# Performance work log

Measured on AMD Instinct MI355X. Metric: run time of the kernel, lower is better.

## Reference

```python
import jax, jax.numpy as jnp
import numpy as np

NUM_BINS = 8
TAIL = 3.0
MBW = 0.001  # min_bin_width
MBH = 0.001  # min_bin_height
MD = 0.001   # min_derivative


def _conv(x, w, b):
    y = jax.lax.conv_general_dilated(x, w, (1, 1), 'SAME',
                                     dimension_numbers=('NCHW', 'OIHW', 'NCHW'))
    return y + b[None, :, None, None]


def _convnet(x, w1, b1, w2, b2, w3, b3):
    h = jax.nn.relu(_conv(x, w1, b1))
    h = jax.nn.relu(_conv(h, w2, b2))
    return _conv(h, w3, b3)


def _rqs_forward(x, uw, uh, ud):
    # x: (N,), uw/uh: (N, num_bins), ud: (N, num_bins-1)
    nb = uw.shape[-1]
    inside = (x >= -TAIL) & (x <= TAIL)
    xin = jnp.clip(x, -TAIL, TAIL)
    # linear tails: pad derivatives so boundary slope == 1
    const = float(np.log(np.exp(1.0 - MD) - 1.0))
    ud = jnp.pad(ud, ((0, 0), (1, 1)), constant_values=const)

    widths = jax.nn.softmax(uw, axis=-1)
    widths = MBW + (1.0 - MBW * nb) * widths
    cumw = jnp.pad(jnp.cumsum(widths, axis=-1), ((0, 0), (1, 0)))
    cumw = 2.0 * TAIL * cumw - TAIL
    cumw = cumw.at[:, 0].set(-TAIL).at[:, -1].set(TAIL)
    widths = cumw[:, 1:] - cumw[:, :-1]

    heights = jax.nn.softmax(uh, axis=-1)
    heights = MBH + (1.0 - MBH * nb) * heights
    cumh = jnp.pad(jnp.cumsum(heights, axis=-1), ((0, 0), (1, 0)))
    cumh = 2.0 * TAIL * cumh - TAIL
    cumh = cumh.at[:, 0].set(-TAIL).at[:, -1].set(TAIL)
    heights = cumh[:, 1:] - cumh[:, :-1]

    deriv = MD + jax.nn.softplus(ud)  # (N, nb+1)

    # searchsorted: locate bin of each element
    idx = jnp.clip(jnp.sum((xin[:, None] >= cumw).astype(jnp.int32), axis=-1) - 1, 0, nb - 1)
    gather = lambda t: jnp.take_along_axis(t, idx[:, None], axis=-1)[:, 0]

    in_cw = gather(cumw)
    in_w = gather(widths)
    in_ch = gather(cumh)
    in_h = gather(heights)
    in_delta = gather(heights / widths)
    d0 = gather(deriv)
    d1 = gather(deriv[:, 1:])

    theta = (xin - in_cw) / in_w
    tom = theta * (1.0 - theta)
    numer = in_h * (in_delta * theta ** 2 + d0 * tom)
    denom = in_delta + (d0 + d1 - 2.0 * in_delta) * tom
    y = in_ch + numer / denom
    dnum = in_delta ** 2 * (d1 * theta ** 2 + 2.0 * in_delta * tom + d0 * (1.0 - theta) ** 2)
    lad = jnp.log(dnum) - 2.0 * jnp.log(denom)

    y = jnp.where(inside, y, x)
    lad = jnp.where(inside, lad, 0.0)
    return y, lad


def setup_inputs() -> dict:
    key = jax.random.key(0)
    ks = jax.random.split(key, 9)
    B, C, H, W = 32, 12, 64, 64
    hidden = 128
    cond_c = C // 3
    out_spline = C * (3 * NUM_BINS - 1)
    x = jax.random.normal(ks[0], (B, C, H, W), dtype=jnp.float32)
    logdet = jnp.zeros((B,), dtype=jnp.float32)
    conditioning = jax.random.normal(ks[1], (B, cond_c, H, W), dtype=jnp.float32)
    w1 = jax.random.normal(ks[2], (hidden, C + cond_c, 3, 3), dtype=jnp.float32) * 0.05
    b1 = jnp.zeros((hidden,), dtype=jnp.float32)
    w2 = jax.random.normal(ks[3], (hidden, hidden, 1, 1), dtype=jnp.float32) * 0.05
    b2 = jnp.zeros((hidden,), dtype=jnp.float32)
    w3 = jax.random.normal(ks[4], (out_spline, hidden, 3, 3), dtype=jnp.float32) * 0.01
    b3 = jnp.zeros((out_spline,), dtype=jnp.float32)
    return {"x": x, "logdet": logdet, "conditioning": conditioning,
            "w1": w1, "b1": b1, "w2": w2, "b2": b2, "w3": w3, "b3": b3}


def reference(x, logdet, conditioning, w1, b1, w2, b2, w3, b3):
    B, C, H, W = x.shape
    net_in = jnp.concatenate([x, conditioning], axis=1)
    params = _convnet(net_in, w1, b1, w2, b2, w3, b3)  # (B, C*(3nb-1), H, W)
    params = params.reshape(B, C, 3 * NUM_BINS - 1, H, W)
    params = params.transpose(0, 1, 3, 4, 2).reshape(B * C * H * W, 3 * NUM_BINS - 1)
    uw = params[:, :NUM_BINS]
    uh = params[:, NUM_BINS:2 * NUM_BINS]
    ud = params[:, 2 * NUM_BINS:]
    y_flat, lad_flat = _rqs_forward(x.reshape(-1), uw, uh, ud)
    y = y_flat.reshape(B, C, H, W)
    logdet_out = logdet + lad_flat.reshape(B, -1).sum(axis=1)
    return y, logdet_out
```

## Files before the change

kernel.cpp:

```cpp
#include <hip/hip_runtime.h>
#include <math.h>


#define NPIX 4096
#define NY   1572864

typedef _Float16 half8 __attribute__((ext_vector_type(8)));
typedef _Float16 half4 __attribute__((ext_vector_type(4)));
typedef float f32x4 __attribute__((ext_vector_type(4)));

#define ASYNC16(gsrc, ldst) \
  __builtin_amdgcn_global_load_lds((const __attribute__((address_space(1))) unsigned int*)(gsrc), \
                                   (__attribute__((address_space(3))) unsigned int*)(ldst), 16, 0, 0)

#define H2P_PLANE 4356
#define H2P_IDX(b, cc, pp) ((((size_t)(b) * 4 + (cc)) * H2P_PLANE + (pp)) << 5)
#define XH_IDX(b, pp) (((size_t)(b) * H2P_PLANE + (pp)) << 5)

__global__ __launch_bounds__(256) void prep_k(
    const float* __restrict__ w1, const float* __restrict__ w2,
    const float* __restrict__ w3, _Float16* __restrict__ w1h,
    _Float16* __restrict__ w2h, _Float16* __restrict__ w3h,
    const float* __restrict__ logdet, float* __restrict__ ld_out)
{
    const int i = blockIdx.x * 256 + threadIdx.x;
    if (i < 36864) {
        int k = i & 31, oc = (i >> 5) & 127, t = i >> 12;
        w1h[i] = (_Float16)((k < 16) ? w1[(oc * 16 + k) * 9 + t] : 0.f);
    }
    if (i < 16384) {
        int km = i & 31, oc = (i >> 5) & 127, ks = i >> 12;
        w2h[i] = (_Float16)w2[oc * 128 + ks * 32 + km];
    }
    {
        int cim = i & 31;
        int oc = (i >> 5) % 288;
        int tc = i / (288 * 32);
        int t = tc >> 2, cc = tc & 3;
        int c = oc / 24, j = oc % 24;
        int ci = cc * 32 + cim;
        float v = (j < 23) ? w3[((c * 23 + j) * 128 + ci) * 9 + t] : 0.f;
        w3h[i] = (_Float16)v;
    }
    if (i < 32) ld_out[i] = logdet[i];
}

__global__ __launch_bounds__(256) void xh_k(
    const float* __restrict__ x, const float* __restrict__ cond,
    _Float16* __restrict__ xh)
{
    const int i = blockIdx.x * 256 + threadIdx.x;
    if (i >= 139392) return;
    const int b = i / H2P_PLANE, pp = i % H2P_PLANE;
    const int pr = pp / 66, pc = pp % 66;
    const bool interior = (pr >= 1) && (pr <= 64) && (pc >= 1) && (pc <= 64);
    _Float16 v[32];
#pragma unroll
    for (int ci = 0; ci < 32; ++ci) v[ci] = (_Float16)0.f;
    if (interior) {
        const int p = (pr - 1) * 64 + (pc - 1);
#pragma unroll
        for (int ci = 0; ci < 12; ++ci)
            v[ci] = (_Float16)x[((size_t)(b * 12 + ci) << 12) + p];
#pragma unroll
        for (int ci = 0; ci < 4; ++ci)
            v[12 + ci] = (_Float16)cond[((size_t)(b * 4 + ci) << 12) + p];
    }
    _Float16* dst = xh + ((size_t)i << 5);
#pragma unroll
    for (int q = 0; q < 4; ++q) *(f32x4*)(dst + q * 8) = *(f32x4*)(v + q * 8);
}

__global__ __launch_bounds__(256) void zring_k(_Float16* __restrict__ h2p)
{
    const int i = blockIdx.x * 256 + threadIdx.x;
    if (i >= 133120) return;
    const int q = i & 3;
    const int rest = i >> 2;
    const int r = rest % 260;
    const int cc = (rest / 260) & 3;
    const int b = rest / 1040;
    int pp;
    if (r < 66)       pp = r;
    else if (r < 132) pp = 65 * 66 + (r - 66);
    else if (r < 196) pp = (r - 131) * 66;
    else              pp = (r - 195) * 66 + 65;
    f32x4 z = {0.f, 0.f, 0.f, 0.f};
    *(f32x4*)(h2p + H2P_IDX(b, cc, pp) + q * 8) = z;
}

__global__ __launch_bounds__(256, 2) void conv1_k(
    const _Float16* __restrict__ xh, const _Float16* __restrict__ w1h,
    const float* __restrict__ b1, _Float16* __restrict__ h1p)
{
    __shared__ __align__(16) char smem[73728];
    const int tid = threadIdx.x;
    const int wv = tid >> 6, lane = tid & 63;
    const int row16 = lane & 15, quad = lane >> 4;
    const int ptile = blockIdx.x;
    const int b = ptile >> 4;
    const int pim0 = (ptile & 15) << 8;
    const int h0 = pim0 >> 6;

#pragma unroll
    for (int k = 0; k < 18; ++k)
        ASYNC16(w1h + (size_t)(k * 256 + tid) * 8, smem + (k * 256 + wv * 64) * 16);

    f32x4 acc[4][8];
#pragma unroll
    for (int pt = 0; pt < 4; ++pt)
#pragma unroll
        for (int ot = 0; ot < 8; ++ot) acc[pt][ot] = (f32x4){0.f, 0.f, 0.f, 0.f};

    __syncthreads();
    const _Float16* wl = (const _Float16*)smem;

    for (int t = 0; t < 9; ++t) {
        const int dy = t / 3, dx = t % 3;
        const int pbase = (h0 + wv + dy) * 66 + dx + row16;
        half8 bf[4], af[8];
#pragma unroll
        for (int pt = 0; pt < 4; ++pt)
            bf[pt] = *(const half8*)(xh + XH_IDX(b, pbase + pt * 16) + quad * 8);
#pragma unroll
        for (int ot = 0; ot < 8; ++ot)
            af[ot] = *(const half8*)(wl + ((t * 128 + ot * 16 + row16) << 5) + quad * 8);
#pragma unroll
        for (int ot = 0; ot < 8; ++ot)
#pragma unroll
            for (int pt = 0; pt < 4; ++pt)
                acc[pt][ot] = __builtin_amdgcn_mfma_f32_16x16x32_f16(af[ot], bf[pt], acc[pt][ot], 0, 0, 0);
    }

    f32x4 bias[8];
#pragma unroll
    for (int ot = 0; ot < 8; ++ot) bias[ot] = *(const f32x4*)(b1 + ot * 16 + quad * 4);
#pragma unroll
    for (int pt = 0; pt < 4; ++pt) {
        const size_t pbase = ((size_t)((b << 12) + pim0 + wv * 64 + pt * 16 + row16)) << 7;
#pragma unroll
        for (int ot = 0; ot < 8; ++ot) {
            half4 v;
#pragma unroll
            for (int r = 0; r < 4; ++r)
                v[r] = (_Float16)fmaxf(acc[pt][ot][r] + bias[ot][r], 0.f);
            *(half4*)(h1p + pbase + ot * 16 + quad * 4) = v;
        }
    }
}

__global__ __launch_bounds__(256, 2) void conv2_k(
    const _Float16* __restrict__ h1p, const _Float16* __restrict__ w2h,
    const float* __restrict__ b2, _Float16* __restrict__ h2p)
{
    __shared__ __align__(16) char smem[33280];
    float* b2l = (float*)(smem + 32768);
    const int tid = threadIdx.x;
    const int wv = tid >> 6, lane = tid & 63;
    const int row16 = lane & 15, quad = lane >> 4;
    const int ptile = blockIdx.x;
    const int b = ptile >> 4;
    const int pim0 = (ptile & 15) << 8;

    if (tid < 128) b2l[tid] = b2[tid];
#pragma unroll
    for (int k = 0; k < 8; ++k) {
        const int c0 = k * 256 + wv * 64;
        ASYNC16(w2h + (size_t)(c0 + lane) * 8, smem + c0 * 16);
    }

    f32x4 acc[4][8];
#pragma unroll
    for (int pt = 0; pt < 4; ++pt)
#pragma unroll
        for (int ot = 0; ot < 8; ++ot) acc[pt][ot] = (f32x4){0.f, 0.f, 0.f, 0.f};

    const int pixbase = (b << 12) + pim0 + wv * 64;
    __syncthreads();

#pragma unroll
    for (int ks = 0; ks < 4; ++ks) {
        half8 bf[4], af[8];
#pragma unroll
        for (int pt = 0; pt < 4; ++pt)
            bf[pt] = *(const half8*)(h1p + ((size_t)(pixbase + pt * 16 + row16) << 7) + ks * 32 + quad * 8);
        const _Float16* wl = (const _Float16*)smem;
#pragma unroll
        for (int ot = 0; ot < 8; ++ot)
            af[ot] = *(const half8*)(wl + ((ks * 128 + ot * 16 + row16) << 5) + quad * 8);
#pragma unroll
        for (int ot = 0; ot < 8; ++ot)
#pragma unroll
            for (int pt = 0; pt < 4; ++pt)
                acc[pt][ot] = __builtin_amdgcn_mfma_f32_16x16x32_f16(af[ot], bf[pt], acc[pt][ot], 0, 0, 0);
    }

#pragma unroll
    for (int pt = 0; pt < 4; ++pt) {
        const int p = pim0 + wv * 64 + pt * 16 + row16;
        const int pp = ((p >> 6) + 1) * 66 + (p & 63) + 1;
#pragma unroll
        for (int ot = 0; ot < 8; ++ot) {
            const int oc0 = ot * 16 + quad * 4;
            half4 v;
#pragma unroll
            for (int r = 0; r < 4; ++r)
                v[r] = (_Float16)fmaxf(acc[pt][ot][r] + b2l[oc0 + r], 0.f);
            *(half4*)(h2p + H2P_IDX(b, oc0 >> 5, pp) + (oc0 & 31)) = v;
        }
    }
}

__device__ __forceinline__ void rqs_eval(const float* prm, float xv,
                                         float& yv_out, float& lad_out)
{
    const float xin = fminf(fmaxf(xv, -3.f), 3.f);

    float mw = prm[0], mh = prm[8];
#pragma unroll
    for (int j = 1; j < 8; ++j) { mw = fmaxf(mw, prm[j]); mh = fmaxf(mh, prm[8 + j]); }
    float ew[8], eh[8];
    float sw = 0.f, sh = 0.f;
#pragma unroll
    for (int j = 0; j < 8; ++j) {
        ew[j] = expf(prm[j] - mw);      sw += ew[j];
        eh[j] = expf(prm[8 + j] - mh);  sh += eh[j];
    }
    const float rw = 1.f / sw, rh = 1.f / sh;

    const float CONST_D = logf(expf(0.999f) - 1.f);

    float cumw = 0.f, cumh = 0.f;
    float cw_lo = -3.f, ch_lo = -3.f;
    float in_cw = 0.f, in_w = 1.f, in_ch = 0.f, in_h = 1.f, sd0 = 0.f, sd1 = 0.f;
#pragma unroll
    for (int i = 0; i < 8; ++i) {
        cumw += fmaf(0.992f, ew[i] * rw, 0.001f);
        cumh += fmaf(0.992f, eh[i] * rh, 0.001f);
        const float cw_hi = (i == 7) ? 3.f : fmaf(6.f, cumw, -3.f);
        const float ch_hi = (i == 7) ? 3.f : fmaf(6.f, cumh, -3.f);
        const bool sel = (xin >= cw_lo) && ((i == 7) || (xin < cw_hi));
        in_cw = sel ? cw_lo : in_cw;
        in_w  = sel ? (cw_hi - cw_lo) : in_w;
        in_ch = sel ? ch_lo : in_ch;
        in_h  = sel ? (ch_hi - ch_lo) : in_h;
        sd0   = sel ? ((i == 0) ? CONST_D : prm[16 + i - 1]) : sd0;
        sd1   = sel ? ((i == 7) ? CONST_D : prm[16 + i]) : sd1;
        cw_lo = cw_hi; ch_lo = ch_hi;
    }

    const float d0 = 0.001f + ((sd0 > 20.f) ? sd0 : log1pf(expf(sd0)));
    const float d1 = 0.001f + ((sd1 > 20.f) ? sd1 : log1pf(expf(sd1)));

    const float delta = in_h / in_w;
    const float theta = (xin - in_cw) / in_w;
    const float omt = 1.f - theta;
    const float tom = theta * omt;
    const float th2 = theta * theta;
    const float numer = in_h * (delta * th2 + d0 * tom);
    const float denom = delta + (d0 + d1 - 2.f * delta) * tom;
    float yv = in_ch + numer / denom;
    const float dnum = delta * delta * (d1 * th2 + 2.f * delta * tom + d0 * omt * omt);
    float lad = logf(dnum) - 2.f * logf(denom);

    const bool inside = (xv >= -3.f) && (xv <= 3.f);
    yv_out = inside ? yv : xv;
    lad_out = inside ? lad : 0.f;
}

__global__ __launch_bounds__(256, 2) void conv3_rqs_k(
    const _Float16* __restrict__ h2p, const _Float16* __restrict__ w3h,
    const float* __restrict__ b3, const float* __restrict__ x,
    float* __restrict__ y, float* __restrict__ ld_out)
{
    __shared__ __align__(16) char smem[44352];
    float* b3l = (float*)(smem + 43776);

    const int tid = threadIdx.x;
    const int wv = tid >> 6, lane = tid & 63;
    const int row16 = lane & 15, quad = lane >> 4;
    const int col = blockIdx.x;
    const int ptile = blockIdx.y;
    const int b = ptile >> 4;
    const int pim0 = (ptile & 15) << 8;
    const int h0 = pim0 >> 6;

    if (tid < 144) {
        const int c = tid / 24, j = tid % 24;
        b3l[tid] = (j < 23) ? b3[(col * 6 + c) * 23 + j] : 0.f;
    }

    f32x4 acc[4][9];
#pragma unroll
    for (int pt = 0; pt < 4; ++pt)
#pragma unroll
        for (int ot = 0; ot < 9; ++ot) acc[pt][ot] = (f32x4){0.f, 0.f, 0.f, 0.f};

    auto stage_wt = [&](int t, int cc, int buf) {
        const _Float16* g = w3h + ((size_t)((t * 4 + cc) * 288 + col * 144) << 5);
        char* wb = smem + 25344 + buf * 9216;
        ASYNC16(g + (size_t)tid * 8, wb + wv * 64 * 16);
        ASYNC16(g + (size_t)(256 + tid) * 8, wb + (256 + wv * 64) * 16);
        if (wv == 0) ASYNC16(g + (size_t)(512 + lane) * 8, wb + 512 * 16);
    };
    auto stage_act = [&](int cc) {
        const _Float16* ga = h2p + H2P_IDX(b, cc, h0 * 66);
#pragma unroll
        for (int k = 0; k < 6; ++k)
            ASYNC16(ga + (size_t)(k * 256 + tid) * 8, smem + (k * 256 + wv * 64) * 16);
        if (wv == 0 && lane < 48)
            ASYNC16(ga + (size_t)(1536 + lane) * 8, smem + 1536 * 16);
    };

    stage_act(0);
    stage_wt(0, 0, 0);

    for (int cc = 0; cc < 4; ++cc) {
        for (int t = 0; t < 9; ++t) {
            const int step = cc * 9 + t;
            __syncthreads();
            if (step + 1 < 36)
                stage_wt((t == 8) ? 0 : t + 1, (t == 8) ? cc + 1 : cc, (step + 1) & 1);
            const _Float16* act = (const _Float16*)smem;
            const _Float16* wt = (const _Float16*)(smem + 25344 + (step & 1) * 9216);
            const int dy = t / 3, dx = t % 3;
            const int lpp = (wv + dy) * 66 + dx + row16;
            half8 bf[4], af[9];
#pragma unroll
            for (int pt = 0; pt < 4; ++pt)
                bf[pt] = *(const half8*)(act + ((lpp + pt * 16) << 5) + quad * 8);
#pragma unroll
            for (int ot = 0; ot < 9; ++ot)
                af[ot] = *(const half8*)(wt + ((ot * 16 + row16) << 5) + quad * 8);
#pragma unroll
            for (int ot = 0; ot < 9; ++ot)
#pragma unroll
                for (int pt = 0; pt < 4; ++pt)
                    acc[pt][ot] = __builtin_amdgcn_mfma_f32_16x16x32_f16(af[ot], bf[pt], acc[pt][ot], 0, 0, 0);
            if (t == 8 && cc < 3) {
                __syncthreads();
                stage_act(cc + 1);
            }
        }
    }
    __syncthreads();

    float* epi = (float*)smem + wv * 2368;
    float lad_acc = 0.f;
#pragma unroll
    for (int pt = 0; pt < 4; ++pt) {
#pragma unroll
        for (int ot = 0; ot < 9; ++ot)
            *(f32x4*)(epi + row16 * 148 + ot * 16 + quad * 4) = acc[pt][ot];
        __syncthreads();
#pragma unroll 1
        for (int pass = 0; pass < 2; ++pass) {
            const int idx = pass * 64 + lane;
            if (idx < 96) {
                const int p16 = idx & 15, c = idx >> 4;
                float prm[23];
#pragma unroll
                for (int j = 0; j < 23; ++j)
                    prm[j] = epi[p16 * 148 + c * 24 + j] + b3l[c * 24 + j];
                const int tpix = wv * 64 + pt * 16 + p16;
                const size_t xi = (((size_t)(b * 12 + col * 6 + c)) << 12) + (pim0 + tpix);
                const float xv = x[xi];
                float yv, lad;
                rqs_eval(prm, xv, yv, lad);
                y[xi] = yv;
                lad_acc += lad;
            }
        }
        __syncthreads();
    }

#pragma unroll
    for (int off = 32; off > 0; off >>= 1) lad_acc += __shfl_down(lad_acc, off);
    if (lane == 0) atomicAdd(&ld_out[b], lad_acc);
}

extern "C" void kernel_launch(void* const* d_in, const int* in_sizes, int n_in,
                              void* d_out, int out_size, void* d_ws, size_t ws_size,
                              hipStream_t stream)
{
    const float* x      = (const float*)d_in[0];
    const float* logdet = (const float*)d_in[1];
    const float* cond   = (const float*)d_in[2];
    const float* w1     = (const float*)d_in[3];
    const float* b1     = (const float*)d_in[4];
    const float* w2     = (const float*)d_in[5];
    const float* b2     = (const float*)d_in[6];
    const float* w3     = (const float*)d_in[7];
    const float* b3     = (const float*)d_in[8];

    char* ws = (char*)d_ws;
    _Float16* h1p = (_Float16*)ws;
    _Float16* h2p = (_Float16*)(ws + 33554432);
    _Float16* xh  = (_Float16*)(ws + 33554432);
    _Float16* w1h = (_Float16*)(ws + 69238784);
    _Float16* w2h = (_Float16*)(ws + 69312512);
    _Float16* w3h = (_Float16*)(ws + 69345280);

    float* y      = (float*)d_out;
    float* ld_out = y + NY;

    prep_k<<<1296, 256, 0, stream>>>(w1, w2, w3, w1h, w2h, w3h, logdet, ld_out);
    xh_k<<<545, 256, 0, stream>>>(x, cond, xh);
    conv1_k<<<512, 256, 0, stream>>>(xh, w1h, b1, h1p);
    zring_k<<<520, 256, 0, stream>>>(h2p);
    conv2_k<<<512, 256, 0, stream>>>(h1p, w2h, b2, h2p);
    conv3_rqs_k<<<dim3(2, 512), 256, 0, stream>>>(h2p, w3h, b3, x, y, ld_out);
}
```

Measured before the change: 240.0 us.

## Split conv3 into three column groups, swizzle LDS, and fuse setup kernels

Merges the activation-packing kernel into the weight-prep kernel and folds the halo-ring zeroing into the conv2 epilogue, removing two launches. conv3 now covers 4 output channel groups per block instead of 6, using 3 grid columns. This shrinks accumulators and LDS so three blocks can fit per CU. An XOR swizzle on the async LDS staging and the fragment reads is added to cut bank conflicts. The cost is more redundant activation loads across the extra column and more blocks overall.

```diff
diff --git a/kernel.cpp b/kernel.cpp
--- a/kernel.cpp
+++ b/kernel.cpp
@@ -13,15 +13,19 @@
   __builtin_amdgcn_global_load_lds((const __attribute__((address_space(1))) unsigned int*)(gsrc), \
                                    (__attribute__((address_space(3))) unsigned int*)(ldst), 16, 0, 0)
 
+__device__ __forceinline__ int swz(int s) { return (s & ~3) | ((s ^ (s >> 2)) & 3); }
+
 #define H2P_PLANE 4356
 #define H2P_IDX(b, cc, pp) ((((size_t)(b) * 4 + (cc)) * H2P_PLANE + (pp)) << 5)
 #define XH_IDX(b, pp) (((size_t)(b) * H2P_PLANE + (pp)) << 5)
 
-__global__ __launch_bounds__(256) void prep_k(
+__global__ __launch_bounds__(256) void setup_k(
     const float* __restrict__ w1, const float* __restrict__ w2,
     const float* __restrict__ w3, _Float16* __restrict__ w1h,
     _Float16* __restrict__ w2h, _Float16* __restrict__ w3h,
-    const float* __restrict__ logdet, float* __restrict__ ld_out)
+    const float* __restrict__ logdet, float* __restrict__ ld_out,
+    const float* __restrict__ x, const float* __restrict__ cond,
+    _Float16* __restrict__ xh)
 {
     const int i = blockIdx.x * 256 + threadIdx.x;
     if (i < 36864) {
@@ -43,50 +47,26 @@
         w3h[i] = (_Float16)v;
     }
     if (i < 32) ld_out[i] = logdet[i];
-}
-
-__global__ __launch_bounds__(256) void xh_k(
-    const float* __restrict__ x, const float* __restrict__ cond,
-    _Float16* __restrict__ xh)
-{
-    const int i = blockIdx.x * 256 + threadIdx.x;
-    if (i >= 139392) return;
-    const int b = i / H2P_PLANE, pp = i % H2P_PLANE;
-    const int pr = pp / 66, pc = pp % 66;
-    const bool interior = (pr >= 1) && (pr <= 64) && (pc >= 1) && (pc <= 64);
-    _Float16 v[32];
-#pragma unroll
-    for (int ci = 0; ci < 32; ++ci) v[ci] = (_Float16)0.f;
-    if (interior) {
-        const int p = (pr - 1) * 64 + (pc - 1);
-#pragma unroll
-        for (int ci = 0; ci < 12; ++ci)
-            v[ci] = (_Float16)x[((size_t)(b * 12 + ci) << 12) + p];
-#pragma unroll
-        for (int ci = 0; ci < 4; ++ci)
-            v[12 + ci] = (_Float16)cond[((size_t)(b * 4 + ci) << 12) + p];
-    }
-    _Float16* dst = xh + ((size_t)i << 5);
-#pragma unroll
-    for (int q = 0; q < 4; ++q) *(f32x4*)(dst + q * 8) = *(f32x4*)(v + q * 8);
-}
-
-__global__ __launch_bounds__(256) void zring_k(_Float16* __restrict__ h2p)
-{
-    const int i = blockIdx.x * 256 + threadIdx.x;
-    if (i >= 133120) return;
-    const int q = i & 3;
-    const int rest = i >> 2;
-    const int r = rest % 260;
-    const int cc = (rest / 260) & 3;
-    const int b = rest / 1040;
-    int pp;
-    if (r < 66)       pp = r;
-    else if (r < 132) pp = 65 * 66 + (r - 66);
-    else if (r < 196) pp = (r - 131) * 66;
-    else              pp = (r - 195) * 66 + 65;
-    f32x4 z = {0.f, 0.f, 0.f, 0.f};
-    *(f32x4*)(h2p + H2P_IDX(b, cc, pp) + q * 8) = z;
+    if (i < 139392) {
+        const int b = i / H2P_PLANE, pp = i % H2P_PLANE;
+        const int pr = pp / 66, pc = pp % 66;
+        const bool interior = (pr >= 1) && (pr <= 64) && (pc >= 1) && (pc <= 64);
+        _Float16 v[32];
+#pragma unroll
+        for (int ci = 0; ci < 32; ++ci) v[ci] = (_Float16)0.f;
+        if (interior) {
+            const int p = (pr - 1) * 64 + (pc - 1);
+#pragma unroll
+            for (int ci = 0; ci < 12; ++ci)
+                v[ci] = (_Float16)x[((size_t)(b * 12 + ci) << 12) + p];
+#pragma unroll
+            for (int ci = 0; ci < 4; ++ci)
+                v[12 + ci] = (_Float16)cond[((size_t)(b * 4 + ci) << 12) + p];
+        }
+        _Float16* dst = xh + ((size_t)i << 5);
+#pragma unroll
+        for (int q = 0; q < 4; ++q) *(f32x4*)(dst + q * 8) = *(f32x4*)(v + q * 8);
+    }
 }
 
 __global__ __launch_bounds__(256, 2) void conv1_k(
@@ -208,6 +188,20 @@
                 v[r] = (_Float16)fmaxf(acc[pt][ot][r] + b2l[oc0 + r], 0.f);
             *(half4*)(h2p + H2P_IDX(b, oc0 >> 5, pp) + (oc0 & 31)) = v;
         }
+    }
+
+    const int gidx = (ptile & 15) * 256 + tid;
+    const f32x4 z = {0.f, 0.f, 0.f, 0.f};
+#pragma unroll 1
+    for (int u = gidx; u < 4160; u += 4096) {
+        const int cc = u / 1040, r4 = u - cc * 1040;
+        const int r = r4 >> 2, q = r4 & 3;
+        int pp;
+        if (r < 66)       pp = r;
+        else if (r < 132) pp = 65 * 66 + (r - 66);
+        else if (r < 196) pp = (r - 131) * 66;
+        else              pp = (r - 195) * 66 + 65;
+        *(f32x4*)(h2p + H2P_IDX(b, cc, pp) + q * 8) = z;
     }
 }
 
@@ -268,13 +262,13 @@
     lad_out = inside ? lad : 0.f;
 }
 
-__global__ __launch_bounds__(256, 2) void conv3_rqs_k(
+__global__ __launch_bounds__(256, 3) void conv3_rqs_k(
     const _Float16* __restrict__ h2p, const _Float16* __restrict__ w3h,
     const float* __restrict__ b3, const float* __restrict__ x,
     float* __restrict__ y, float* __restrict__ ld_out)
 {
-    __shared__ __align__(16) char smem[44352];
-    float* b3l = (float*)(smem + 43776);
+    __shared__ __align__(16) char smem[38016];
+    float* b3l = (float*)(smem + 37632);
 
     const int tid = threadIdx.x;
     const int wv = tid >> 6, lane = tid & 63;
@@ -285,35 +279,37 @@
     const int pim0 = (ptile & 15) << 8;
     const int h0 = pim0 >> 6;
 
-    if (tid < 144) {
+    if (tid < 96) {
         const int c = tid / 24, j = tid % 24;
-        b3l[tid] = (j < 23) ? b3[(col * 6 + c) * 23 + j] : 0.f;
-    }
-
-    f32x4 acc[4][9];
+        b3l[tid] = (j < 23) ? b3[(col * 4 + c) * 23 + j] : 0.f;
+    }
+
+    f32x4 acc[4][6];
 #pragma unroll
     for (int pt = 0; pt < 4; ++pt)
 #pragma unroll
-        for (int ot = 0; ot < 9; ++ot) acc[pt][ot] = (f32x4){0.f, 0.f, 0.f, 0.f};
+        for (int ot = 0; ot < 6; ++ot) acc[pt][ot] = (f32x4){0.f, 0.f, 0.f, 0.f};
 
     auto stage_wt = [&](int t, int cc, int buf) {
-        const _Float16* g = w3h + ((size_t)((t * 4 + cc) * 288 + col * 144) << 5);
-        char* wb = smem + 25344 + buf * 9216;
-        ASYNC16(g + (size_t)tid * 8, wb + wv * 64 * 16);
-        ASYNC16(g + (size_t)(256 + tid) * 8, wb + (256 + wv * 64) * 16);
-        if (wv == 0) ASYNC16(g + (size_t)(512 + lane) * 8, wb + 512 * 16);
+        const _Float16* g = w3h + ((size_t)((t * 4 + cc) * 288 + col * 96) << 5);
+        char* wb = smem + 25344 + buf * 6144;
+        ASYNC16(g + (size_t)swz(tid) * 8, wb + wv * 64 * 16);
+        if (wv < 2)
+            ASYNC16(g + (size_t)swz(256 + wv * 64 + lane) * 8, wb + (256 + wv * 64) * 16);
     };
     auto stage_act = [&](int cc) {
         const _Float16* ga = h2p + H2P_IDX(b, cc, h0 * 66);
 #pragma unroll
         for (int k = 0; k < 6; ++k)
-            ASYNC16(ga + (size_t)(k * 256 + tid) * 8, smem + (k * 256 + wv * 64) * 16);
+            ASYNC16(ga + (size_t)swz(k * 256 + tid) * 8, smem + (k * 256 + wv * 64) * 16);
         if (wv == 0 && lane < 48)
-            ASYNC16(ga + (size_t)(1536 + lane) * 8, smem + 1536 * 16);
+            ASYNC16(ga + (size_t)swz(1536 + lane) * 8, smem + 1536 * 16);
     };
 
     stage_act(0);
     stage_wt(0, 0, 0);
+
+    const int qxw = (quad ^ (row16 & 3)) << 3;
 
     for (int cc = 0; cc < 4; ++cc) {
         for (int t = 0; t < 9; ++t) {
@@ -322,18 +318,19 @@
             if (step + 1 < 36)
                 stage_wt((t == 8) ? 0 : t + 1, (t == 8) ? cc + 1 : cc, (step + 1) & 1);
             const _Float16* act = (const _Float16*)smem;
-            const _Float16* wt = (const _Float16*)(smem + 25344 + (step & 1) * 9216);
+            const _Float16* wt = (const _Float16*)(smem + 25344 + (step & 1) * 6144);
             const int dy = t / 3, dx = t % 3;
             const int lpp = (wv + dy) * 66 + dx + row16;
-            half8 bf[4], af[9];
+            const int qxa = (quad ^ (lpp & 3)) << 3;
+            half8 bf[4], af[6];
 #pragma unroll
             for (int pt = 0; pt < 4; ++pt)
-                bf[pt] = *(const half8*)(act + ((lpp + pt * 16) << 5) + quad * 8);
-#pragma unroll
-            for (int ot = 0; ot < 9; ++ot)
-                af[ot] = *(const half8*)(wt + ((ot * 16 + row16) << 5) + quad * 8);
-#pragma unroll
-            for (int ot = 0; ot < 9; ++ot)
+                bf[pt] = *(const half8*)(act + ((lpp + pt * 16) << 5) + qxa);
+#pragma unroll
+            for (int ot = 0; ot < 6; ++ot)
+                af[ot] = *(const half8*)(wt + ((ot * 16 + row16) << 5) + qxw);
+#pragma unroll
+            for (int ot = 0; ot < 6; ++ot)
 #pragma unroll
                 for (int pt = 0; pt < 4; ++pt)
                     acc[pt][ot] = __builtin_amdgcn_mfma_f32_16x16x32_f16(af[ot], bf[pt], acc[pt][ot], 0, 0, 0);
@@ -345,31 +342,27 @@
     }
     __syncthreads();
 
-    float* epi = (float*)smem + wv * 2368;
+    float* epi = (float*)smem + wv * 1600;
     float lad_acc = 0.f;
 #pragma unroll
     for (int pt = 0; pt < 4; ++pt) {
 #pragma unroll
-        for (int ot = 0; ot < 9; ++ot)
-            *(f32x4*)(epi + row16 * 148 + ot * 16 + quad * 4) = acc[pt][ot];
+        for (int ot = 0; ot < 6; ++ot)
+            *(f32x4*)(epi + row16 * 100 + ot * 16 + quad * 4) = acc[pt][ot];
         __syncthreads();
-#pragma unroll 1
-        for (int pass = 0; pass < 2; ++pass) {
-            const int idx = pass * 64 + lane;
-            if (idx < 96) {
-                const int p16 = idx & 15, c = idx >> 4;
-                float prm[23];
-#pragma unroll
-                for (int j = 0; j < 23; ++j)
-                    prm[j] = epi[p16 * 148 + c * 24 + j] + b3l[c * 24 + j];
-                const int tpix = wv * 64 + pt * 16 + p16;
-                const size_t xi = (((size_t)(b * 12 + col * 6 + c)) << 12) + (pim0 + tpix);
-                const float xv = x[xi];
-                float yv, lad;
-                rqs_eval(prm, xv, yv, lad);
-                y[xi] = yv;
-                lad_acc += lad;
-            }
+        {
+            const int p16 = lane & 15, c = lane >> 4;
+            float prm[23];
+#pragma unroll
+            for (int j = 0; j < 23; ++j)
+                prm[j] = epi[p16 * 100 + c * 24 + j] + b3l[c * 24 + j];
+            const int tpix = wv * 64 + pt * 16 + p16;
+            const size_t xi = (((size_t)(b * 12 + col * 4 + c)) << 12) + (pim0 + tpix);
+            const float xv = x[xi];
+            float yv, lad;
+            rqs_eval(prm, xv, yv, lad);
+            y[xi] = yv;
+            lad_acc += lad;
         }
         __syncthreads();
     }
@@ -404,10 +397,9 @@
     float* y      = (float*)d_out;
     float* ld_out = y + NY;
 
-    prep_k<<<1296, 256, 0, stream>>>(w1, w2, w3, w1h, w2h, w3h, logdet, ld_out);
-    xh_k<<<545, 256, 0, stream>>>(x, cond, xh);
+    setup_k<<<1296, 256, 0, stream>>>(w1, w2, w3, w1h, w2h, w3h, logdet, ld_out,
+                                      x, cond, xh);
     conv1_k<<<512, 256, 0, stream>>>(xh, w1h, b1, h1p);
-    zring_k<<<520, 256, 0, stream>>>(h2p);
     conv2_k<<<512, 256, 0, stream>>>(h1p, w2h, b2, h2p);
-    conv3_rqs_k<<<dim3(2, 512), 256, 0, stream>>>(h2p, w3h, b3, x, y, ld_out);
-}
+    conv3_rqs_k<<<dim3(3, 512), 256, 0, stream>>>(h2p, w3h, b3, x, y, ld_out);
+}
```

Result: slower. 269.2 us (+12.2%).
